# Performance work log

Measured on AMD Instinct MI355X. Metric: run time of the kernel, lower is better.

The kernel has to match this reference:

```python
import jax, jax.numpy as jnp
import numpy as np

N_NODES = 50000
TAU = 1.0 + (1.0 / 1000.0) * (0.1 - 1.0)  # anneal step 1 -> 0.9991


def setup_inputs() -> dict:
    key = jax.random.key(0)
    ks = jax.random.split(key, 8)
    N, F, H, E, K = N_NODES, 128, 128, 800000, 5
    node_features = jax.random.normal(ks[0], (N, F), dtype=jnp.float32)
    src = jnp.sort(jax.random.randint(ks[1], (E,), 0, N, dtype=jnp.int32))
    dst = jax.random.randint(ks[2], (E,), 0, N, dtype=jnp.int32)
    u_noise = jax.random.uniform(ks[3], (K, E), dtype=jnp.float32,
                                 minval=1e-6, maxval=1.0 - 1e-6)
    # MLP params: Linear(2F -> H), ReLU, Linear(H -> 1)
    W1 = jax.random.normal(ks[4], (2 * F, H), dtype=jnp.float32) / np.sqrt(2 * F)
    b1 = jnp.zeros((H,), dtype=jnp.float32)
    W2 = jax.random.normal(ks[5], (H, 1), dtype=jnp.float32) / np.sqrt(H)
    b2 = jnp.zeros((1,), dtype=jnp.float32)
    return {"node_features": node_features, "W1": W1, "b1": b1,
            "W2": W2, "b2": b2, "u_noise": u_noise, "src": src, "dst": dst}


def reference(node_features, W1, b1, W2, b2, u_noise, src, dst):
    N = N_NODES
    F = node_features.shape[1]
    # per-edge MLP on concat([x_u, x_v]) without materializing the (E, 2F) concat
    x_u = node_features[src]                      # (E, F)
    x_v = node_features[dst]                      # (E, F)
    h = jax.nn.relu(x_u @ W1[:F] + x_v @ W1[F:] + b1)   # (E, H)
    z = (h @ W2 + b2)[:, 0]                       # (E,)
    # per-node (segment) log-softmax over each node's neighbor edges
    zmax = jax.ops.segment_max(z, src, num_segments=N)
    ze = z - zmax[src]
    denom = jax.ops.segment_sum(jnp.exp(ze), src, num_segments=N)
    log_pi = ze - jnp.log(denom)[src]             # (E,)
    # k rounds of Gumbel-softmax sampling
    g = -jnp.log(-jnp.log(u_noise))               # (K, E)
    scores = (log_pi[None, :] + g) / TAU          # (K, E)

    def seg_softmax(s):
        m = jax.ops.segment_max(s, src, num_segments=N)
        e = jnp.exp(s - m[src])
        return e / jax.ops.segment_sum(e, src, num_segments=N)[src]

    def seg_argmax_dst(s):
        m = jax.ops.segment_max(s, src, num_segments=N)
        hit = s >= m[src]
        sel = jax.ops.segment_max(jnp.where(hit, dst, -1), src, num_segments=N)
        return sel  # (N,) selected neighbor per node, per round

    soft = jax.vmap(seg_softmax)(scores)          # (K, E) gumbel-softmax probs
    selected = jax.vmap(seg_argmax_dst)(scores)   # (K, N) sampled neighbor ids
    return selected, soft
```

## Files before the change

kernel.cpp:

```cpp
#include <hip/hip_runtime.h>

#define FEAT 128
#define HID  128
#define XS_STRIDE 68

__global__ __launch_bounds__(256) void gemm_ab(
    const float* __restrict__ X, const float* __restrict__ W1,
    float* __restrict__ A, float* __restrict__ B, int N) {
  __shared__ float xs[FEAT * XS_STRIDE];
  __shared__ float ws[32 * HID];
  const int t = threadIdx.x;
  const int n0 = blockIdx.x * 64;

  {
    const int nl = t >> 2;
    const int fi = t & 3;
    const int n = n0 + nl;
    const bool ok = n < N;
    const float* xrow = X + (size_t)n * FEAT;
#pragma unroll
    for (int rep = 0; rep < 8; ++rep) {
      const int f0 = fi * 4 + rep * 16;
      float4 v = make_float4(0.f, 0.f, 0.f, 0.f);
      if (ok) v = *(const float4*)(xrow + f0);
      xs[(f0 + 0) * XS_STRIDE + nl] = v.x;
      xs[(f0 + 1) * XS_STRIDE + nl] = v.y;
      xs[(f0 + 2) * XS_STRIDE + nl] = v.z;
      xs[(f0 + 3) * XS_STRIDE + nl] = v.w;
    }
  }

  const int tn = t & 15;
  const int tc = t >> 4;

  for (int pass = 0; pass < 2; ++pass) {
    float acc[4][8];
#pragma unroll
    for (int r = 0; r < 4; ++r)
#pragma unroll
      for (int c = 0; c < 8; ++c) acc[r][c] = 0.f;

    for (int kc = 0; kc < 4; ++kc) {
      __syncthreads();
#pragma unroll
      for (int rep = 0; rep < 4; ++rep) {
        const int idx = rep * 256 + t;
        const int r = idx >> 5;
        const int c4 = (idx & 31) << 2;
        *(float4*)&ws[r * HID + c4] =
            *(const float4*)(W1 + (size_t)(pass * FEAT + kc * 32 + r) * HID + c4);
      }
      __syncthreads();

#pragma unroll 4
      for (int k = 0; k < 32; ++k) {
        const float4 xv = *(const float4*)&xs[(kc * 32 + k) * XS_STRIDE + tn * 4];
        const float4 w0 = *(const float4*)&ws[k * HID + tc * 8];
        const float4 w1 = *(const float4*)&ws[k * HID + tc * 8 + 4];
        const float xr[4] = {xv.x, xv.y, xv.z, xv.w};
#pragma unroll
        for (int r = 0; r < 4; ++r) {
          acc[r][0] = fmaf(xr[r], w0.x, acc[r][0]);
          acc[r][1] = fmaf(xr[r], w0.y, acc[r][1]);
          acc[r][2] = fmaf(xr[r], w0.z, acc[r][2]);
          acc[r][3] = fmaf(xr[r], w0.w, acc[r][3]);
          acc[r][4] = fmaf(xr[r], w1.x, acc[r][4]);
          acc[r][5] = fmaf(xr[r], w1.y, acc[r][5]);
          acc[r][6] = fmaf(xr[r], w1.z, acc[r][6]);
          acc[r][7] = fmaf(xr[r], w1.w, acc[r][7]);
        }
      }
    }

    float* O = pass ? B : A;
#pragma unroll
    for (int r = 0; r < 4; ++r) {
      const int n = n0 + tn * 4 + r;
      if (n < N) {
        *(float4*)(O + (size_t)n * HID + tc * 8) =
            make_float4(acc[r][0], acc[r][1], acc[r][2], acc[r][3]);
        *(float4*)(O + (size_t)n * HID + tc * 8 + 4) =
            make_float4(acc[r][4], acc[r][5], acc[r][6], acc[r][7]);
      }
    }
  }
}

__global__ __launch_bounds__(256) void row_offsets(
    const int* __restrict__ src, int* __restrict__ rs, int N, int E) {
  const int n = blockIdx.x * 256 + threadIdx.x;
  if (n > N) return;
  int lo = 0, hi = E;
  while (lo < hi) {
    const int mid = (lo + hi) >> 1;
    if (src[mid] < n) lo = mid + 1; else hi = mid;
  }
  rs[n] = lo;
}

__global__ __launch_bounds__(256) void edge_z(
    const float* __restrict__ A, const float* __restrict__ B,
    const float* __restrict__ b1, const float* __restrict__ W2,
    const float* __restrict__ b2, const int* __restrict__ src,
    const int* __restrict__ dst, float* __restrict__ z, int E) {
  const int g = threadIdx.x >> 4;
  const int l = threadIdx.x & 15;
  const int e0 = blockIdx.x * 32 + g * 2;
  if (e0 >= E) return;
  const int e1 = e0 + 1;
  const bool has1 = e1 < E;

  const int u0 = src[e0], v0 = dst[e0];
  const int u1 = has1 ? src[e1] : u0;
  const int v1 = has1 ? dst[e1] : v0;

  const float4* Au0 = (const float4*)(A + (size_t)u0 * HID) + l * 2;
  const float4* Bv0 = (const float4*)(B + (size_t)v0 * HID) + l * 2;
  const float4* Au1 = (const float4*)(A + (size_t)u1 * HID) + l * 2;
  const float4* Bv1 = (const float4*)(B + (size_t)v1 * HID) + l * 2;

  const float4 a00 = Au0[0], a01 = Au0[1];
  const float4 b00 = Bv0[0], b01 = Bv0[1];
  const float4 a10 = Au1[0], a11 = Au1[1];
  const float4 b10 = Bv1[0], b11 = Bv1[1];

  const float4 c0 = *(const float4*)(b1 + l * 8);
  const float4 c1 = *(const float4*)(b1 + l * 8 + 4);
  const float4 w0 = *(const float4*)(W2 + l * 8);
  const float4 w1 = *(const float4*)(W2 + l * 8 + 4);
  const float bias2 = b2[0];

  float p0 = fmaxf(a00.x + b00.x + c0.x, 0.f) * w0.x
           + fmaxf(a00.y + b00.y + c0.y, 0.f) * w0.y
           + fmaxf(a00.z + b00.z + c0.z, 0.f) * w0.z
           + fmaxf(a00.w + b00.w + c0.w, 0.f) * w0.w
           + fmaxf(a01.x + b01.x + c1.x, 0.f) * w1.x
           + fmaxf(a01.y + b01.y + c1.y, 0.f) * w1.y
           + fmaxf(a01.z + b01.z + c1.z, 0.f) * w1.z
           + fmaxf(a01.w + b01.w + c1.w, 0.f) * w1.w;
  float p1 = fmaxf(a10.x + b10.x + c0.x, 0.f) * w0.x
           + fmaxf(a10.y + b10.y + c0.y, 0.f) * w0.y
           + fmaxf(a10.z + b10.z + c0.z, 0.f) * w0.z
           + fmaxf(a10.w + b10.w + c0.w, 0.f) * w0.w
           + fmaxf(a11.x + b11.x + c1.x, 0.f) * w1.x
           + fmaxf(a11.y + b11.y + c1.y, 0.f) * w1.y
           + fmaxf(a11.z + b11.z + c1.z, 0.f) * w1.z
           + fmaxf(a11.w + b11.w + c1.w, 0.f) * w1.w;

#pragma unroll
  for (int m = 8; m >= 1; m >>= 1) {
    p0 += __shfl_xor(p0, m);
    p1 += __shfl_xor(p1, m);
  }
  if (l == 0) {
    z[e0] = p0 + bias2;
    if (has1) z[e1] = p1 + bias2;
  }
}

__global__ __launch_bounds__(256) void seg_sample(
    const float* __restrict__ z, const float* __restrict__ U,
    const int* __restrict__ dst, const int* __restrict__ rs,
    float* __restrict__ out_sel, float* __restrict__ out_soft,
    int N, int E, int K) {
  const int n = blockIdx.x * 4 + (threadIdx.x >> 6);
  if (n >= N) return;
  const int lane = threadIdx.x & 63;
  const int start = rs[n];
  const int deg = rs[n + 1] - start;
  const float TAU = 0.9991f;

  if (deg == 0) {
    if (lane == 0)
      for (int k = 0; k < K; ++k) out_sel[(size_t)k * N + n] = -2147483648.0f;
    return;
  }

  if (deg <= 64) {
    const bool act = lane < deg;
    const int e = start + (act ? lane : 0);
    const float zv = act ? z[e] : -INFINITY;
    const int d = act ? dst[e] : -1;
    float zmax = zv;
#pragma unroll
    for (int m = 32; m >= 1; m >>= 1) zmax = fmaxf(zmax, __shfl_xor(zmax, m));
    float den = act ? expf(zv - zmax) : 0.f;
#pragma unroll
    for (int m = 32; m >= 1; m >>= 1) den += __shfl_xor(den, m);
    const float lp = (zv - zmax) - logf(den);

    for (int k = 0; k < K; ++k) {
      float s = -INFINITY;
      if (act) {
        const float uu = U[(size_t)k * E + e];
        const float g = -logf(-logf(uu));
        s = (lp + g) / TAU;
      }
      float m2 = s;
#pragma unroll
      for (int m = 32; m >= 1; m >>= 1) m2 = fmaxf(m2, __shfl_xor(m2, m));
      float ex = act ? expf(s - m2) : 0.f;
      float d2 = ex;
#pragma unroll
      for (int m = 32; m >= 1; m >>= 1) d2 += __shfl_xor(d2, m);
      int cand = (act && s >= m2) ? d : -1;
#pragma unroll
      for (int m = 32; m >= 1; m >>= 1) cand = max(cand, __shfl_xor(cand, m));
      if (lane == 0) out_sel[(size_t)k * N + n] = (float)cand;
      if (act) out_soft[(size_t)k * E + e] = ex / d2;
    }
  } else {
    float zmax = -INFINITY;
    for (int c = lane; c < deg; c += 64) zmax = fmaxf(zmax, z[start + c]);
#pragma unroll
    for (int m = 32; m >= 1; m >>= 1) zmax = fmaxf(zmax, __shfl_xor(zmax, m));
    float den = 0.f;
    for (int c = lane; c < deg; c += 64) den += expf(z[start + c] - zmax);
#pragma unroll
    for (int m = 32; m >= 1; m >>= 1) den += __shfl_xor(den, m);
    const float logd = logf(den);

    for (int k = 0; k < K; ++k) {
      float m2 = -INFINITY;
      for (int c = lane; c < deg; c += 64) {
        const int e = start + c;
        const float g = -logf(-logf(U[(size_t)k * E + e]));
        const float s = ((z[e] - zmax) - logd + g) / TAU;
        m2 = fmaxf(m2, s);
      }
#pragma unroll
      for (int m = 32; m >= 1; m >>= 1) m2 = fmaxf(m2, __shfl_xor(m2, m));
      float d2 = 0.f;
      int cand = -1;
      for (int c = lane; c < deg; c += 64) {
        const int e = start + c;
        const float g = -logf(-logf(U[(size_t)k * E + e]));
        const float s = ((z[e] - zmax) - logd + g) / TAU;
        d2 += expf(s - m2);
        if (s >= m2) cand = max(cand, dst[e]);
      }
#pragma unroll
      for (int m = 32; m >= 1; m >>= 1) d2 += __shfl_xor(d2, m);
#pragma unroll
      for (int m = 32; m >= 1; m >>= 1) cand = max(cand, __shfl_xor(cand, m));
      if (lane == 0) out_sel[(size_t)k * N + n] = (float)cand;
      for (int c = lane; c < deg; c += 64) {
        const int e = start + c;
        const float g = -logf(-logf(U[(size_t)k * E + e]));
        const float s = ((z[e] - zmax) - logd + g) / TAU;
        out_soft[(size_t)k * E + e] = expf(s - m2) / d2;
      }
    }
  }
}

extern "C" void kernel_launch(void* const* d_in, const int* in_sizes, int n_in,
                              void* d_out, int out_size, void* d_ws, size_t ws_size,
                              hipStream_t stream) {
  const float* X  = (const float*)d_in[0];
  const float* W1 = (const float*)d_in[1];
  const float* b1 = (const float*)d_in[2];
  const float* W2 = (const float*)d_in[3];
  const float* b2 = (const float*)d_in[4];
  const float* U  = (const float*)d_in[5];
  const int* src  = (const int*)d_in[6];
  const int* dst  = (const int*)d_in[7];
  const int E = in_sizes[6];
  const int K = in_sizes[5] / E;
  const int N = in_sizes[0] / FEAT;

  float* A = (float*)d_ws;
  float* B = A + (size_t)N * HID;
  float* z = B + (size_t)N * HID;
  int* rs  = (int*)(z + E);

  float* out_sel  = (float*)d_out;
  float* out_soft = (float*)d_out + (size_t)K * N;

  hipLaunchKernelGGL(gemm_ab, dim3((N + 63) / 64), dim3(256), 0, stream,
                     X, W1, A, B, N);
  hipLaunchKernelGGL(row_offsets, dim3((N + 256) / 256), dim3(256), 0, stream,
                     src, rs, N, E);
  hipLaunchKernelGGL(edge_z, dim3((E + 31) / 32), dim3(256), 0, stream,
                     A, B, b1, W2, b2, src, dst, z, E);
  hipLaunchKernelGGL(seg_sample, dim3((N + 3) / 4), dim3(256), 0, stream,
                     z, U, dst, rs, out_sel, out_soft, N, E, K);
}
```

Measured before the change: 265.5 us.

## Retile node GEMM over output columns and pack two nodes per wave in sampling

The node-feature GEMM now tiles 128 nodes by 64 output columns on a 2D grid. It streams X in 32-wide k-chunks instead of staging the whole row block, which raises block count and cuts shared-memory use. The sampling kernel gives each half-wave its own node when every degree in the wave is at most 32, with a fallback to the old full-wave path otherwise. In the small-degree path the max pass is dropped by computing exp directly from the log-softmax score, using fast intrinsics and a combined argmax reduction. This trades numerical safety (no max subtraction, fast log/exp/rcp) for fewer reductions and better lane utilisation.

```diff
diff --git a/kernel.cpp b/kernel.cpp
--- a/kernel.cpp
+++ b/kernel.cpp
@@ -2,86 +2,81 @@
 
 #define FEAT 128
 #define HID  128
-#define XS_STRIDE 68
+#define XS_S 132
 
 __global__ __launch_bounds__(256) void gemm_ab(
     const float* __restrict__ X, const float* __restrict__ W1,
     float* __restrict__ A, float* __restrict__ B, int N) {
-  __shared__ float xs[FEAT * XS_STRIDE];
-  __shared__ float ws[32 * HID];
+  __shared__ float xs[32 * XS_S];
+  __shared__ float ws[32 * 64];
   const int t = threadIdx.x;
-  const int n0 = blockIdx.x * 64;
-
-  {
-    const int nl = t >> 2;
-    const int fi = t & 3;
-    const int n = n0 + nl;
-    const bool ok = n < N;
-    const float* xrow = X + (size_t)n * FEAT;
-#pragma unroll
-    for (int rep = 0; rep < 8; ++rep) {
-      const int f0 = fi * 4 + rep * 16;
+  const int n0 = blockIdx.x * 128;
+  const int j0 = blockIdx.y * 64;
+  const float* Wbase = W1 + (j0 < 128 ? j0 : 128 * HID + (j0 - 128));
+  float* Obase = (j0 < 128) ? (A + j0) : (B + (j0 - 128));
+
+  const int tn = t & 31;
+  const int tc = t >> 5;
+
+  float acc[4][8];
+#pragma unroll
+  for (int r = 0; r < 4; ++r)
+#pragma unroll
+    for (int c = 0; c < 8; ++c) acc[r][c] = 0.f;
+
+  const int ln = t >> 3;
+  const int lf = (t & 7) * 4;
+
+  for (int kc = 0; kc < 4; ++kc) {
+    __syncthreads();
+#pragma unroll
+    for (int rep = 0; rep < 4; ++rep) {
+      const int nl = ln + rep * 32;
+      const int n = n0 + nl;
       float4 v = make_float4(0.f, 0.f, 0.f, 0.f);
-      if (ok) v = *(const float4*)(xrow + f0);
-      xs[(f0 + 0) * XS_STRIDE + nl] = v.x;
-      xs[(f0 + 1) * XS_STRIDE + nl] = v.y;
-      xs[(f0 + 2) * XS_STRIDE + nl] = v.z;
-      xs[(f0 + 3) * XS_STRIDE + nl] = v.w;
-    }
-  }
-
-  const int tn = t & 15;
-  const int tc = t >> 4;
-
-  for (int pass = 0; pass < 2; ++pass) {
-    float acc[4][8];
-#pragma unroll
-    for (int r = 0; r < 4; ++r)
-#pragma unroll
-      for (int c = 0; c < 8; ++c) acc[r][c] = 0.f;
-
-    for (int kc = 0; kc < 4; ++kc) {
-      __syncthreads();
-#pragma unroll
-      for (int rep = 0; rep < 4; ++rep) {
-        const int idx = rep * 256 + t;
-        const int r = idx >> 5;
-        const int c4 = (idx & 31) << 2;
-        *(float4*)&ws[r * HID + c4] =
-            *(const float4*)(W1 + (size_t)(pass * FEAT + kc * 32 + r) * HID + c4);
-      }
-      __syncthreads();
-
-#pragma unroll 4
-      for (int k = 0; k < 32; ++k) {
-        const float4 xv = *(const float4*)&xs[(kc * 32 + k) * XS_STRIDE + tn * 4];
-        const float4 w0 = *(const float4*)&ws[k * HID + tc * 8];
-        const float4 w1 = *(const float4*)&ws[k * HID + tc * 8 + 4];
-        const float xr[4] = {xv.x, xv.y, xv.z, xv.w};
-#pragma unroll
-        for (int r = 0; r < 4; ++r) {
-          acc[r][0] = fmaf(xr[r], w0.x, acc[r][0]);
-          acc[r][1] = fmaf(xr[r], w0.y, acc[r][1]);
-          acc[r][2] = fmaf(xr[r], w0.z, acc[r][2]);
-          acc[r][3] = fmaf(xr[r], w0.w, acc[r][3]);
-          acc[r][4] = fmaf(xr[r], w1.x, acc[r][4]);
-          acc[r][5] = fmaf(xr[r], w1.y, acc[r][5]);
-          acc[r][6] = fmaf(xr[r], w1.z, acc[r][6]);
-          acc[r][7] = fmaf(xr[r], w1.w, acc[r][7]);
-        }
-      }
-    }
-
-    float* O = pass ? B : A;
-#pragma unroll
-    for (int r = 0; r < 4; ++r) {
-      const int n = n0 + tn * 4 + r;
-      if (n < N) {
-        *(float4*)(O + (size_t)n * HID + tc * 8) =
-            make_float4(acc[r][0], acc[r][1], acc[r][2], acc[r][3]);
-        *(float4*)(O + (size_t)n * HID + tc * 8 + 4) =
-            make_float4(acc[r][4], acc[r][5], acc[r][6], acc[r][7]);
-      }
+      if (n < N) v = *(const float4*)(X + (size_t)n * FEAT + kc * 32 + lf);
+      xs[(lf + 0) * XS_S + nl] = v.x;
+      xs[(lf + 1) * XS_S + nl] = v.y;
+      xs[(lf + 2) * XS_S + nl] = v.z;
+      xs[(lf + 3) * XS_S + nl] = v.w;
+    }
+#pragma unroll
+    for (int rep = 0; rep < 2; ++rep) {
+      const int idx = rep * 256 + t;
+      const int r = idx >> 4;
+      const int c4 = (idx & 15) * 4;
+      *(float4*)&ws[r * 64 + c4] =
+          *(const float4*)(Wbase + (size_t)(kc * 32 + r) * HID + c4);
+    }
+    __syncthreads();
+
+#pragma unroll 8
+    for (int k = 0; k < 32; ++k) {
+      const float4 xv = *(const float4*)&xs[k * XS_S + tn * 4];
+      const float4 w0 = *(const float4*)&ws[k * 64 + tc * 8];
+      const float4 w1 = *(const float4*)&ws[k * 64 + tc * 8 + 4];
+      const float xr[4] = {xv.x, xv.y, xv.z, xv.w};
+#pragma unroll
+      for (int r = 0; r < 4; ++r) {
+        acc[r][0] = fmaf(xr[r], w0.x, acc[r][0]);
+        acc[r][1] = fmaf(xr[r], w0.y, acc[r][1]);
+        acc[r][2] = fmaf(xr[r], w0.z, acc[r][2]);
+        acc[r][3] = fmaf(xr[r], w0.w, acc[r][3]);
+        acc[r][4] = fmaf(xr[r], w1.x, acc[r][4]);
+        acc[r][5] = fmaf(xr[r], w1.y, acc[r][5]);
+        acc[r][6] = fmaf(xr[r], w1.z, acc[r][6]);
+        acc[r][7] = fmaf(xr[r], w1.w, acc[r][7]);
+      }
+    }
+  }
+
+#pragma unroll
+  for (int r = 0; r < 4; ++r) {
+    const int n = n0 + tn * 4 + r;
+    if (n < N) {
+      float* o = Obase + (size_t)n * HID + tc * 8;
+      *(float4*)o = make_float4(acc[r][0], acc[r][1], acc[r][2], acc[r][3]);
+      *(float4*)(o + 4) = make_float4(acc[r][4], acc[r][5], acc[r][6], acc[r][7]);
     }
   }
 }
@@ -163,79 +158,101 @@
     const int* __restrict__ dst, const int* __restrict__ rs,
     float* __restrict__ out_sel, float* __restrict__ out_soft,
     int N, int E, int K) {
-  const int n = blockIdx.x * 4 + (threadIdx.x >> 6);
-  if (n >= N) return;
-  const int lane = threadIdx.x & 63;
-  const int start = rs[n];
-  const int deg = rs[n + 1] - start;
-  const float TAU = 0.9991f;
-
-  if (deg == 0) {
-    if (lane == 0)
-      for (int k = 0; k < K; ++k) out_sel[(size_t)k * N + n] = -2147483648.0f;
-    return;
-  }
-
-  if (deg <= 64) {
-    const bool act = lane < deg;
-    const int e = start + (act ? lane : 0);
+  const int t = threadIdx.x;
+  const int lane = t & 63;
+  const int half = lane >> 5;
+  const int hl = lane & 31;
+  const int n = blockIdx.x * 8 + (t >> 6) * 2 + half;
+  const float INVTAU = 1.0f / 0.9991f;
+
+  int start = 0, deg = 0;
+  if (n < N) { start = rs[n]; deg = rs[n + 1] - start; }
+
+  if (__all(deg <= 32)) {
+    if (n >= N) return;
+    if (deg == 0) {
+      if (hl == 0)
+        for (int k = 0; k < K; ++k) out_sel[(size_t)k * N + n] = -2147483648.0f;
+      return;
+    }
+    const bool act = hl < deg;
+    const int e = start + (act ? hl : 0);
     const float zv = act ? z[e] : -INFINITY;
     const int d = act ? dst[e] : -1;
+
     float zmax = zv;
 #pragma unroll
-    for (int m = 32; m >= 1; m >>= 1) zmax = fmaxf(zmax, __shfl_xor(zmax, m));
-    float den = act ? expf(zv - zmax) : 0.f;
-#pragma unroll
-    for (int m = 32; m >= 1; m >>= 1) den += __shfl_xor(den, m);
-    const float lp = (zv - zmax) - logf(den);
+    for (int m = 16; m >= 1; m >>= 1) zmax = fmaxf(zmax, __shfl_xor(zmax, m));
+    float den = act ? __expf(zv - zmax) : 0.f;
+#pragma unroll
+    for (int m = 16; m >= 1; m >>= 1) den += __shfl_xor(den, m);
+    const float lpb = (zv - zmax) - __logf(den);
 
     for (int k = 0; k < K; ++k) {
-      float s = -INFINITY;
+      float ex = 0.f;
       if (act) {
         const float uu = U[(size_t)k * E + e];
-        const float g = -logf(-logf(uu));
-        s = (lp + g) / TAU;
-      }
-      float m2 = s;
-#pragma unroll
-      for (int m = 32; m >= 1; m >>= 1) m2 = fmaxf(m2, __shfl_xor(m2, m));
-      float ex = act ? expf(s - m2) : 0.f;
+        const float t2 = -__logf(uu);
+        const float g = -__logf(t2);
+        ex = __expf((lpb + g) * INVTAU);
+      }
       float d2 = ex;
-#pragma unroll
-      for (int m = 32; m >= 1; m >>= 1) d2 += __shfl_xor(d2, m);
-      int cand = (act && s >= m2) ? d : -1;
-#pragma unroll
-      for (int m = 32; m >= 1; m >>= 1) cand = max(cand, __shfl_xor(cand, m));
-      if (lane == 0) out_sel[(size_t)k * N + n] = (float)cand;
-      if (act) out_soft[(size_t)k * E + e] = ex / d2;
-    }
-  } else {
+      float mx = ex;
+      int md = d;
+#pragma unroll
+      for (int m = 16; m >= 1; m >>= 1) {
+        d2 += __shfl_xor(d2, m);
+        const float ox = __shfl_xor(mx, m);
+        const int od = __shfl_xor(md, m);
+        if (ox > mx) { mx = ox; md = od; }
+        else if (ox == mx) md = max(md, od);
+      }
+      if (hl == 0) out_sel[(size_t)k * N + n] = (float)md;
+      if (act) {
+        const float inv = __builtin_amdgcn_rcpf(d2);
+        out_soft[(size_t)k * E + e] = ex * inv;
+      }
+    }
+    return;
+  }
+
+  const int wbase = blockIdx.x * 8 + (t >> 6) * 2;
+  for (int j = 0; j < 2; ++j) {
+    const int nn = wbase + j;
+    if (nn >= N) continue;
+    const int st = rs[nn];
+    const int dg = rs[nn + 1] - st;
+    if (dg == 0) {
+      if (lane == 0)
+        for (int k = 0; k < K; ++k) out_sel[(size_t)k * N + nn] = -2147483648.0f;
+      continue;
+    }
     float zmax = -INFINITY;
-    for (int c = lane; c < deg; c += 64) zmax = fmaxf(zmax, z[start + c]);
+    for (int c = lane; c < dg; c += 64) zmax = fmaxf(zmax, z[st + c]);
 #pragma unroll
     for (int m = 32; m >= 1; m >>= 1) zmax = fmaxf(zmax, __shfl_xor(zmax, m));
     float den = 0.f;
-    for (int c = lane; c < deg; c += 64) den += expf(z[start + c] - zmax);
+    for (int c = lane; c < dg; c += 64) den += expf(z[st + c] - zmax);
 #pragma unroll
     for (int m = 32; m >= 1; m >>= 1) den += __shfl_xor(den, m);
     const float logd = logf(den);
 
     for (int k = 0; k < K; ++k) {
       float m2 = -INFINITY;
-      for (int c = lane; c < deg; c += 64) {
-        const int e = start + c;
+      for (int c = lane; c < dg; c += 64) {
+        const int e = st + c;
         const float g = -logf(-logf(U[(size_t)k * E + e]));
-        const float s = ((z[e] - zmax) - logd + g) / TAU;
+        const float s = ((z[e] - zmax) - logd + g) * INVTAU;
         m2 = fmaxf(m2, s);
       }
 #pragma unroll
       for (int m = 32; m >= 1; m >>= 1) m2 = fmaxf(m2, __shfl_xor(m2, m));
       float d2 = 0.f;
       int cand = -1;
-      for (int c = lane; c < deg; c += 64) {
-        const int e = start + c;
+      for (int c = lane; c < dg; c += 64) {
+        const int e = st + c;
         const float g = -logf(-logf(U[(size_t)k * E + e]));
-        const float s = ((z[e] - zmax) - logd + g) / TAU;
+        const float s = ((z[e] - zmax) - logd + g) * INVTAU;
         d2 += expf(s - m2);
         if (s >= m2) cand = max(cand, dst[e]);
       }
@@ -243,11 +260,11 @@
       for (int m = 32; m >= 1; m >>= 1) d2 += __shfl_xor(d2, m);
 #pragma unroll
       for (int m = 32; m >= 1; m >>= 1) cand = max(cand, __shfl_xor(cand, m));
-      if (lane == 0) out_sel[(size_t)k * N + n] = (float)cand;
-      for (int c = lane; c < deg; c += 64) {
-        const int e = start + c;
+      if (lane == 0) out_sel[(size_t)k * N + nn] = (float)cand;
+      for (int c = lane; c < dg; c += 64) {
+        const int e = st + c;
         const float g = -logf(-logf(U[(size_t)k * E + e]));
-        const float s = ((z[e] - zmax) - logd + g) / TAU;
+        const float s = ((z[e] - zmax) - logd + g) * INVTAU;
         out_soft[(size_t)k * E + e] = expf(s - m2) / d2;
       }
     }
@@ -277,12 +294,12 @@
   float* out_sel  = (float*)d_out;
   float* out_soft = (float*)d_out + (size_t)K * N;
 
-  hipLaunchKernelGGL(gemm_ab, dim3((N + 63) / 64), dim3(256), 0, stream,
+  hipLaunchKernelGGL(gemm_ab, dim3((N + 127) / 128, 4), dim3(256), 0, stream,
                      X, W1, A, B, N);
   hipLaunchKernelGGL(row_offsets, dim3((N + 256) / 256), dim3(256), 0, stream,
                      src, rs, N, E);
   hipLaunchKernelGGL(edge_z, dim3((E + 31) / 32), dim3(256), 0, stream,
                      A, B, b1, W2, b2, src, dst, z, E);
-  hipLaunchKernelGGL(seg_sample, dim3((N + 3) / 4), dim3(256), 0, stream,
+  hipLaunchKernelGGL(seg_sample, dim3((N + 7) / 8), dim3(256), 0, stream,
                      z, U, dst, rs, out_sel, out_soft, N, E, K);
 }
```

Result: faster. 237.4 us (-10.6%).
